# Performance work log

Measured on AMD Instinct MI355X. Metric: run time of the kernel, lower is better.

Reference implementation:

```python
import jax, jax.numpy as jnp
import numpy as np

N = 50000        # nodes
E = 800000       # edges (before self-loops)
IN_C = 256
OUT_C = 64
HEADS = 4
NEG_SLOPE = 0.2  # PyG GATConv default


def setup_inputs() -> dict:
    key = jax.random.key(0)
    k0, k1, k2, k3, k4 = jax.random.split(key, 5)
    x = jax.random.normal(k0, (N, IN_C), jnp.float32)
    edge_index = jax.random.randint(k1, (2, E), 0, N, dtype=jnp.int32)
    W = jax.random.normal(k2, (IN_C, HEADS * OUT_C), jnp.float32) * (1.0 / np.sqrt(IN_C))
    att_src = jax.random.normal(k3, (HEADS, OUT_C), jnp.float32) * 0.1
    att_dst = jax.random.normal(k4, (HEADS, OUT_C), jnp.float32) * 0.1
    bias = jnp.zeros((OUT_C,), jnp.float32)
    return {"x": x, "edge_index": edge_index, "W": W,
            "att_src": att_src, "att_dst": att_dst, "bias": bias}


def reference(x, edge_index, W, att_src, att_dst, bias):
    n = x.shape[0]
    # PyG GATConv default add_self_loops=True
    loop = jnp.arange(n, dtype=edge_index.dtype)
    src = jnp.concatenate([edge_index[0], loop])  # [E+N]
    dst = jnp.concatenate([edge_index[1], loop])  # [E+N]

    h = (x @ W).reshape(n, HEADS, OUT_C)                    # [N,H,C]
    a_src = jnp.einsum('nhc,hc->nh', h, att_src)            # [N,H]
    a_dst = jnp.einsum('nhc,hc->nh', h, att_dst)            # [N,H]

    e = jax.nn.leaky_relu(a_src[src] + a_dst[dst], NEG_SLOPE)   # [E',H]
    # segment softmax over edges grouped by destination node
    m = jax.lax.stop_gradient(jax.ops.segment_max(e, dst, num_segments=n))  # [N,H]
    ex = jnp.exp(e - m[dst])
    denom = jax.ops.segment_sum(ex, dst, num_segments=n)    # [N,H]
    alpha = ex / (denom[dst] + 1e-16)                       # [E',H]

    out = jax.ops.segment_sum(alpha[:, :, None] * h[src], dst, num_segments=n)  # [N,H,C]
    # concat=False -> mean over heads, then bias
    return out.mean(axis=1) + bias
```

## Files before the change

kernel.cpp:

```cpp
#include <hip/hip_runtime.h>
#include <hip/hip_bf16.h>

#define INC   256
#define HEADS 4
#define OUTC  64
#define NEG_SLOPE 0.2f
#define CAP   5120
#define EPB_A 2048

typedef __attribute__((ext_vector_type(8))) short  fragA;
typedef __attribute__((ext_vector_type(4))) float  f32x4;

__device__ __forceinline__ float bf2f(unsigned short u) {
    union { unsigned int i; float f; } v; v.i = ((unsigned int)u) << 16; return v.f;
}
__device__ __forceinline__ unsigned short f2bf(float x) {
    __hip_bfloat16 b = __float2bfloat16(x);
    return *reinterpret_cast<unsigned short*>(&b);
}

__global__ __launch_bounds__(256) void wt_zero_kernel(const float* __restrict__ W,
                                                      unsigned short* __restrict__ Wt,
                                                      int* __restrict__ btail, int nbuck)
{
    int idx = blockIdx.x * 256 + threadIdx.x;
    int k = idx >> 8, c = idx & 255;
    Wt[c * 256 + k] = f2bf(W[k * 256 + c]);
    if (idx < nbuck) btail[idx] = 0;
}

__global__ __launch_bounds__(256, 2) void gemm_passA(
    const float* __restrict__ A,
    const unsigned short* __restrict__ Wt,
    const float* __restrict__ att_src,
    const float* __restrict__ att_dst,
    unsigned short* __restrict__ H2,
    float* __restrict__ a_srcO,
    float* __restrict__ a_dstO,
    int M,
    const int* __restrict__ src, const int* __restrict__ dst,
    int* __restrict__ btail,
    int2* __restrict__ bucketbuf,
    int E, int nbA)
{
    __shared__ __align__(16) unsigned short As[64 * 256];
    const int tid = threadIdx.x;

    if ((int)blockIdx.x < nbA) {
        char* sm = (char*)As;
        int* lhist = (int*)sm;
        int* lrankc = (int*)(sm + 1024);
        int* gbase  = (int*)(sm + 2048);
        lhist[tid] = 0; lrankc[tid] = 0;
        __syncthreads();
        int e0 = blockIdx.x * EPB_A;
        int e1 = e0 + EPB_A; if (e1 > E) e1 = E;
        for (int e = e0 + tid; e < e1; e += 256)
            atomicAdd(&lhist[dst[e] >> 8], 1);
        __syncthreads();
        {
            int c = lhist[tid];
            gbase[tid] = (c > 0) ? atomicAdd(&btail[tid], c) : 0;
        }
        __syncthreads();
        for (int e = e0 + tid; e < e1; e += 256) {
            int s = src[e], d = dst[e];
            int b = d >> 8;
            int r = atomicAdd(&lrankc[b], 1);
            bucketbuf[(size_t)b * CAP + gbase[b] + r] = make_int2(s, d);
        }
        return;
    }

    const int lane = tid & 63;
    const int wave = tid >> 6;
    const int row0 = ((int)blockIdx.x - nbA) * 64;
    const int g   = lane >> 4;
    const int r16 = lane & 15;

    fragA b[4][8];
    {
        const unsigned short* wp = Wt + (size_t)(wave * 64) * 256;
        #pragma unroll
        for (int nn = 0; nn < 4; ++nn)
            #pragma unroll
            for (int kk = 0; kk < 8; ++kk)
                b[nn][kk] = *(const fragA*)(wp + (size_t)(nn * 16 + r16) * 256 + kk * 32 + g * 8);
    }

    #pragma unroll
    for (int i = 0; i < 16; ++i) {
        int f   = i * 256 + tid;
        int row = f >> 6;
        int q   = f & 63;
        int gr  = row0 + row;
        float4 v = (gr < M) ? *(const float4*)(A + (size_t)gr * INC + q * 4)
                            : make_float4(0.f, 0.f, 0.f, 0.f);
        ushort4 u;
        u.x = f2bf(v.x); u.y = f2bf(v.y); u.z = f2bf(v.z); u.w = f2bf(v.w);
        int byte = (row << 9) + (q << 3);
        byte ^= (row & 7) << 4;
        *(ushort4*)((char*)As + byte) = u;
    }
    __syncthreads();

    f32x4 acc[4][4] = {};
    #pragma unroll
    for (int kk = 0; kk < 8; ++kk) {
        fragA a[4];
        #pragma unroll
        for (int m = 0; m < 4; ++m) {
            int row  = m * 16 + r16;
            int byte = (row << 9) + ((kk * 32 + g * 8) << 1);
            byte ^= (row & 7) << 4;
            a[m] = *(const fragA*)((const char*)As + byte);
        }
        #pragma unroll
        for (int m = 0; m < 4; ++m)
            #pragma unroll
            for (int nn = 0; nn < 4; ++nn)
                acc[m][nn] = __builtin_amdgcn_mfma_f32_16x16x32_bf16(
                    a[m], b[nn][kk], acc[m][nn], 0, 0, 0);
    }

    #pragma unroll
    for (int m = 0; m < 4; ++m) {
        #pragma unroll
        for (int nn = 0; nn < 4; ++nn) {
            int gcol = wave * 64 + nn * 16 + r16;
            #pragma unroll
            for (int r = 0; r < 4; ++r) {
                int grow = row0 + m * 16 + g * 4 + r;
                if (grow < M)
                    H2[(size_t)grow * (HEADS * OUTC) + gcol] = f2bf(acc[m][nn][r]);
            }
        }
    }

    {
        float as_att[4], ad_att[4];
        #pragma unroll
        for (int nn = 0; nn < 4; ++nn) {
            as_att[nn] = att_src[wave * 64 + nn * 16 + r16];
            ad_att[nn] = att_dst[wave * 64 + nn * 16 + r16];
        }
        float sv[4][4], dv[4][4];
        #pragma unroll
        for (int m = 0; m < 4; ++m)
            #pragma unroll
            for (int r = 0; r < 4; ++r) {
                float s = 0.f, d = 0.f;
                #pragma unroll
                for (int nn = 0; nn < 4; ++nn) {
                    s = fmaf(acc[m][nn][r], as_att[nn], s);
                    d = fmaf(acc[m][nn][r], ad_att[nn], d);
                }
                sv[m][r] = s; dv[m][r] = d;
            }
        #pragma unroll
        for (int off = 1; off < 16; off <<= 1) {
            #pragma unroll
            for (int m = 0; m < 4; ++m)
                #pragma unroll
                for (int r = 0; r < 4; ++r) {
                    sv[m][r] += __shfl_xor(sv[m][r], off, 64);
                    dv[m][r] += __shfl_xor(dv[m][r], off, 64);
                }
        }
        #pragma unroll
        for (int m = 0; m < 4; ++m)
            #pragma unroll
            for (int r = 0; r < 4; ++r) {
                if (r16 == m * 4 + r) {
                    int grow = row0 + m * 16 + g * 4 + r;
                    if (grow < M) {
                        a_srcO[(size_t)grow * HEADS + wave] = sv[m][r];
                        a_dstO[(size_t)grow * HEADS + wave] = dv[m][r];
                    }
                }
            }
    }
}

__global__ __launch_bounds__(256) void passB_kernel(const int2* __restrict__ bucketbuf,
                                                    const int* __restrict__ btail,
                                                    int* __restrict__ offsets,
                                                    int* __restrict__ esrc,
                                                    int N, int E)
{
    __shared__ int lcnt[256];
    __shared__ int red[256];
    __shared__ unsigned short lrank[CAP];
    const int b = blockIdx.x, t = threadIdx.x;

    int s0 = 0;
    for (int j = t; j < b; j += 256) s0 += btail[j];
    red[t] = s0;
    __syncthreads();
    for (int off = 128; off > 0; off >>= 1) {
        if (t < off) red[t] += red[t + off];
        __syncthreads();
    }
    const int baseg = red[0];
    const int cnt = btail[b];
    __syncthreads();

    lcnt[t] = 0;
    __syncthreads();
    const int2* bb = bucketbuf + (size_t)b * CAP;
    for (int i = t; i < cnt; i += 256)
        lrank[i] = (unsigned short)atomicAdd(&lcnt[bb[i].y & 255], 1);
    __syncthreads();

    int v = lcnt[t];
    red[t] = v;
    __syncthreads();
    for (int off = 1; off < 256; off <<= 1) {
        int x = (t >= off) ? red[t - off] : 0;
        __syncthreads();
        red[t] += x;
        __syncthreads();
    }
    int excl = red[t] - v;
    lcnt[t] = excl;
    int node = b * 256 + t;
    if (node < N) offsets[node] = baseg + excl;
    if (b == 0 && t == 0) offsets[N] = E;
    __syncthreads();

    for (int i = t; i < cnt; i += 256) {
        int2 sd = bb[i];
        int slot = baseg + lcnt[sd.y & 255] + lrank[i];
        esrc[slot] = sd.x;
    }
}

__global__ __launch_bounds__(128) void fused_agg_kernel(
    const unsigned short* __restrict__ h2,
    const float* __restrict__ a_src,
    const float* __restrict__ a_dst,
    const int*   __restrict__ offsets,
    const int*   __restrict__ esrc,
    const float* __restrict__ bias,
    float*       __restrict__ out,
    int n)
{
    int i    = (int)((blockIdx.x * blockDim.x + threadIdx.x) >> 6);
    int lane = threadIdx.x & 63;
    if (i >= n) return;
    const int h  = lane >> 4;
    const int cg = lane & 15;

    const float ad = a_dst[(size_t)i * HEADS + h];
    const unsigned short* h2p = h2 + lane * 4;

    float acc0, acc1, acc2, acc3, l;
    {
        float as = a_src[(size_t)i * HEADS + h];
        float e = as + ad; e = e > 0.f ? e : NEG_SLOPE * e;
        float p = __expf(e);
        ushort4 v = *(const ushort4*)(h2p + (size_t)i * 256);
        l = p;
        acc0 = p * bf2f(v.x);
        acc1 = p * bf2f(v.y);
        acc2 = p * bf2f(v.z);
        acc3 = p * bf2f(v.w);
    }

#define EDGE_BODY(S, AS)                                                     \
    {                                                                        \
        float e_ = (AS) + ad; e_ = e_ > 0.f ? e_ : NEG_SLOPE * e_;           \
        float p_ = __expf(e_);                                               \
        ushort4 v_ = *(const ushort4*)(h2p + (size_t)(S) * 256);             \
        l += p_;                                                             \
        acc0 = fmaf(p_, bf2f(v_.x), acc0);                                   \
        acc1 = fmaf(p_, bf2f(v_.y), acc1);                                   \
        acc2 = fmaf(p_, bf2f(v_.z), acc2);                                   \
        acc3 = fmaf(p_, bf2f(v_.w), acc3);                                   \
    }

    int beg = offsets[i], end = offsets[i + 1];
    int j = beg;
    for (; j < end && (j & 3); ++j) {
        int s = esrc[j];
        float as = a_src[(size_t)s * HEADS + h];
        EDGE_BODY(s, as);
    }
    for (; j + 3 < end; j += 4) {
        int4 ea = *(const int4*)(esrc + j);
        float as0 = a_src[(size_t)ea.x * HEADS + h];
        float as1 = a_src[(size_t)ea.y * HEADS + h];
        float as2 = a_src[(size_t)ea.z * HEADS + h];
        float as3 = a_src[(size_t)ea.w * HEADS + h];
        ushort4 v0 = *(const ushort4*)(h2p + (size_t)ea.x * 256);
        ushort4 v1 = *(const ushort4*)(h2p + (size_t)ea.y * 256);
        ushort4 v2 = *(const ushort4*)(h2p + (size_t)ea.z * 256);
        ushort4 v3 = *(const ushort4*)(h2p + (size_t)ea.w * 256);
        float e0 = as0 + ad; e0 = e0 > 0.f ? e0 : NEG_SLOPE * e0; float p0 = __expf(e0);
        float e1 = as1 + ad; e1 = e1 > 0.f ? e1 : NEG_SLOPE * e1; float p1 = __expf(e1);
        float e2 = as2 + ad; e2 = e2 > 0.f ? e2 : NEG_SLOPE * e2; float p2 = __expf(e2);
        float e3 = as3 + ad; e3 = e3 > 0.f ? e3 : NEG_SLOPE * e3; float p3 = __expf(e3);
        l += (p0 + p1) + (p2 + p3);
        acc0 = fmaf(p0, bf2f(v0.x), acc0);
        acc1 = fmaf(p0, bf2f(v0.y), acc1);
        acc2 = fmaf(p0, bf2f(v0.z), acc2);
        acc3 = fmaf(p0, bf2f(v0.w), acc3);
        acc0 = fmaf(p1, bf2f(v1.x), acc0);
        acc1 = fmaf(p1, bf2f(v1.y), acc1);
        acc2 = fmaf(p1, bf2f(v1.z), acc2);
        acc3 = fmaf(p1, bf2f(v1.w), acc3);
        acc0 = fmaf(p2, bf2f(v2.x), acc0);
        acc1 = fmaf(p2, bf2f(v2.y), acc1);
        acc2 = fmaf(p2, bf2f(v2.z), acc2);
        acc3 = fmaf(p2, bf2f(v2.w), acc3);
        acc0 = fmaf(p3, bf2f(v3.x), acc0);
        acc1 = fmaf(p3, bf2f(v3.y), acc1);
        acc2 = fmaf(p3, bf2f(v3.z), acc2);
        acc3 = fmaf(p3, bf2f(v3.w), acc3);
    }
    for (; j < end; ++j) {
        int s = esrc[j];
        float as = a_src[(size_t)s * HEADS + h];
        EDGE_BODY(s, as);
    }
#undef EDGE_BODY

    float inv = 1.f / (l + 1e-16f);
    float r0 = acc0 * inv, r1 = acc1 * inv, r2 = acc2 * inv, r3 = acc3 * inv;

    r0 += __shfl_xor(r0, 16, 64); r0 += __shfl_xor(r0, 32, 64);
    r1 += __shfl_xor(r1, 16, 64); r1 += __shfl_xor(r1, 32, 64);
    r2 += __shfl_xor(r2, 16, 64); r2 += __shfl_xor(r2, 32, 64);
    r3 += __shfl_xor(r3, 16, 64); r3 += __shfl_xor(r3, 32, 64);

    if (lane < 16) {
        float4 b4 = *(const float4*)(bias + cg * 4);
        float4 o;
        o.x = 0.25f * r0 + b4.x;
        o.y = 0.25f * r1 + b4.y;
        o.z = 0.25f * r2 + b4.z;
        o.w = 0.25f * r3 + b4.w;
        *(float4*)(out + (size_t)i * OUTC + cg * 4) = o;
    }
}

extern "C" void kernel_launch(void* const* d_in, const int* in_sizes, int n_in,
                              void* d_out, int out_size, void* d_ws, size_t ws_size,
                              hipStream_t stream)
{
    (void)n_in; (void)out_size; (void)ws_size;
    const float* x       = (const float*)d_in[0];
    const int*   edge    = (const int*)d_in[1];
    const float* W       = (const float*)d_in[2];
    const float* att_src = (const float*)d_in[3];
    const float* att_dst = (const float*)d_in[4];
    const float* bias    = (const float*)d_in[5];
    float* out = (float*)d_out;

    const int N = in_sizes[0] / INC;
    const int E = in_sizes[1] / 2;
    const int* srcA = edge;
    const int* dstA = edge + E;
    const int nbuck = (N + 255) / 256;
    const int nbA   = (E + EPB_A - 1) / EPB_A;

    char* ws = (char*)d_ws;
    unsigned short* h2 = (unsigned short*)ws; ws += (size_t)N * (HEADS * OUTC) * sizeof(unsigned short);
    unsigned short* Wt = (unsigned short*)ws; ws += (size_t)256 * 256 * sizeof(unsigned short);
    float* a_src  = (float*)ws; ws += (size_t)N * HEADS * sizeof(float);
    float* a_dst  = (float*)ws; ws += (size_t)N * HEADS * sizeof(float);
    int* offsets  = (int*)ws;   ws += (size_t)(N + 1) * sizeof(int) + 12;
    int* btail    = (int*)ws;   ws += (size_t)256 * sizeof(int);
    int2* bucketbuf = (int2*)ws; ws += (size_t)nbuck * CAP * sizeof(int2);
    int* esrc     = (int*)ws;   ws += (size_t)E * sizeof(int);

    wt_zero_kernel<<<256, 256, 0, stream>>>(W, Wt, btail, nbuck);

    gemm_passA<<<nbA + (N + 63) / 64, 256, 0, stream>>>(
        x, Wt, att_src, att_dst, h2, a_src, a_dst, N,
        srcA, dstA, btail, bucketbuf, E, nbA);

    passB_kernel<<<nbuck, 256, 0, stream>>>(bucketbuf, btail, offsets, esrc, N, E);

    fused_agg_kernel<<<(N + 1) / 2, 128, 0, stream>>>(h2, a_src, a_dst, offsets, esrc,
                                                      bias, out, N);
}
```

Measured before the change: 135.7 us.

## Replace global atomic bucket reservation with separate histogram and scan kernels

The per-block destination histogram and the global atomicAdd on the bucket tails are split out of the fused GEMM/bucketing kernel. They become a histogram kernel plus a per-bucket exclusive scan kernel, so each bucketing block gets precomputed, deterministic base offsets. This removes the contended global atomics and one pass over dst from the bucketing blocks. In exchange it adds two kernel launches, an extra read of dst, and blockhist/blockbase traffic, all on the critical path before the GEMM launch.

```diff
diff --git a/kernel.cpp b/kernel.cpp
--- a/kernel.cpp
+++ b/kernel.cpp
@@ -19,14 +19,47 @@
     return *reinterpret_cast<unsigned short*>(&b);
 }
 
-__global__ __launch_bounds__(256) void wt_zero_kernel(const float* __restrict__ W,
-                                                      unsigned short* __restrict__ Wt,
-                                                      int* __restrict__ btail, int nbuck)
+__global__ __launch_bounds__(256) void wt_kernel(const float* __restrict__ W,
+                                                 unsigned short* __restrict__ Wt)
 {
     int idx = blockIdx.x * 256 + threadIdx.x;
     int k = idx >> 8, c = idx & 255;
     Wt[c * 256 + k] = f2bf(W[k * 256 + c]);
-    if (idx < nbuck) btail[idx] = 0;
+}
+
+__global__ __launch_bounds__(256) void passA1_kernel(const int* __restrict__ dst,
+                                                     int* __restrict__ blockhist,
+                                                     int E)
+{
+    __shared__ int lh[256];
+    const int t = threadIdx.x, blk = blockIdx.x;
+    lh[t] = 0;
+    __syncthreads();
+    int e0 = blk * EPB_A;
+    int e1 = e0 + EPB_A; if (e1 > E) e1 = E;
+    for (int e = e0 + t; e < e1; e += 256)
+        atomicAdd(&lh[dst[e] >> 8], 1);
+    __syncthreads();
+    blockhist[blk * 256 + t] = lh[t];
+}
+
+__global__ __launch_bounds__(512) void scanb_kernel(const int* __restrict__ blockhist,
+                                                    int* __restrict__ blockbase,
+                                                    int* __restrict__ btail, int nbA)
+{
+    __shared__ int tmp[512];
+    const int t = threadIdx.x, b = blockIdx.x;
+    int v = (t < nbA) ? blockhist[t * 256 + b] : 0;
+    tmp[t] = v;
+    __syncthreads();
+    for (int off = 1; off < 512; off <<= 1) {
+        int x = (t >= off) ? tmp[t - off] : 0;
+        __syncthreads();
+        tmp[t] += x;
+        __syncthreads();
+    }
+    if (t < nbA) blockbase[t * 256 + b] = tmp[t] - v;
+    if (t == nbA - 1) btail[b] = tmp[t];
 }
 
 __global__ __launch_bounds__(256, 2) void gemm_passA(
@@ -39,7 +72,7 @@
     float* __restrict__ a_dstO,
     int M,
     const int* __restrict__ src, const int* __restrict__ dst,
-    int* __restrict__ btail,
+    const int* __restrict__ blockbase,
     int2* __restrict__ bucketbuf,
     int E, int nbA)
 {
@@ -48,26 +81,18 @@
 
     if ((int)blockIdx.x < nbA) {
         char* sm = (char*)As;
-        int* lhist = (int*)sm;
-        int* lrankc = (int*)(sm + 1024);
-        int* gbase  = (int*)(sm + 2048);
-        lhist[tid] = 0; lrankc[tid] = 0;
+        int* lrankc = (int*)sm;
+        int* lbase  = (int*)(sm + 1024);
+        lrankc[tid] = 0;
+        lbase[tid]  = blockbase[(size_t)blockIdx.x * 256 + tid];
         __syncthreads();
         int e0 = blockIdx.x * EPB_A;
         int e1 = e0 + EPB_A; if (e1 > E) e1 = E;
-        for (int e = e0 + tid; e < e1; e += 256)
-            atomicAdd(&lhist[dst[e] >> 8], 1);
-        __syncthreads();
-        {
-            int c = lhist[tid];
-            gbase[tid] = (c > 0) ? atomicAdd(&btail[tid], c) : 0;
-        }
-        __syncthreads();
         for (int e = e0 + tid; e < e1; e += 256) {
             int s = src[e], d = dst[e];
             int b = d >> 8;
             int r = atomicAdd(&lrankc[b], 1);
-            bucketbuf[(size_t)b * CAP + gbase[b] + r] = make_int2(s, d);
+            bucketbuf[(size_t)b * CAP + lbase[b] + r] = make_int2(s, d);
         }
         return;
     }
@@ -371,14 +396,19 @@
     float* a_dst  = (float*)ws; ws += (size_t)N * HEADS * sizeof(float);
     int* offsets  = (int*)ws;   ws += (size_t)(N + 1) * sizeof(int) + 12;
     int* btail    = (int*)ws;   ws += (size_t)256 * sizeof(int);
+    int* blockhist= (int*)ws;   ws += (size_t)nbA * 256 * sizeof(int);
+    int* blockbase= (int*)ws;   ws += (size_t)nbA * 256 * sizeof(int);
     int2* bucketbuf = (int2*)ws; ws += (size_t)nbuck * CAP * sizeof(int2);
     int* esrc     = (int*)ws;   ws += (size_t)E * sizeof(int);
 
-    wt_zero_kernel<<<256, 256, 0, stream>>>(W, Wt, btail, nbuck);
+    wt_kernel<<<256, 256, 0, stream>>>(W, Wt);
+
+    passA1_kernel<<<nbA, 256, 0, stream>>>(dstA, blockhist, E);
+    scanb_kernel<<<256, 512, 0, stream>>>(blockhist, blockbase, btail, nbA);
 
     gemm_passA<<<nbA + (N + 63) / 64, 256, 0, stream>>>(
         x, Wt, att_src, att_dst, h2, a_src, a_dst, N,
-        srcA, dstA, btail, bucketbuf, E, nbA);
+        srcA, dstA, blockbase, bucketbuf, E, nbA);
 
     passB_kernel<<<nbuck, 256, 0, stream>>>(bucketbuf, btail, offsets, esrc, N, E);
 
```

New measurement: 136.5 us. About the same (+0.6%).

## Load GEMM A fragments directly from global, drop LDS staging and preloaded B

Applied to the files above, without the earlier changes.

The GEMM part of the fused kernel no longer converts a 64x256 tile of x into swizzled LDS. Each wave instead loads and converts its A fragments straight from global memory per k-step, and loads W fragments per k-step rather than preloading all 32 into registers. This removes the LDS tile, its barrier and most register pressure, so more blocks can be resident once the min-blocks launch bound is dropped. The cost is that all 4 waves of a block re-read the same A rows from global/L2 with strided 32-byte loads. Edges per histogram block are also doubled to cut block count and global atomics.

```diff
diff --git a/kernel.cpp b/kernel.cpp
--- a/kernel.cpp
+++ b/kernel.cpp
@@ -6,7 +6,7 @@
 #define OUTC  64
 #define NEG_SLOPE 0.2f
 #define CAP   5120
-#define EPB_A 2048
+#define EPB_A 4096
 
 typedef __attribute__((ext_vector_type(8))) short  fragA;
 typedef __attribute__((ext_vector_type(4))) float  f32x4;
@@ -18,18 +18,28 @@
     __hip_bfloat16 b = __float2bfloat16(x);
     return *reinterpret_cast<unsigned short*>(&b);
 }
+__device__ __forceinline__ fragA load_cvt(const float* __restrict__ p) {
+    float4 lo = *(const float4*)p;
+    float4 hi = *(const float4*)(p + 4);
+    fragA f;
+    f[0] = (short)f2bf(lo.x); f[1] = (short)f2bf(lo.y);
+    f[2] = (short)f2bf(lo.z); f[3] = (short)f2bf(lo.w);
+    f[4] = (short)f2bf(hi.x); f[5] = (short)f2bf(hi.y);
+    f[6] = (short)f2bf(hi.z); f[7] = (short)f2bf(hi.w);
+    return f;
+}
 
 __global__ __launch_bounds__(256) void wt_zero_kernel(const float* __restrict__ W,
                                                       unsigned short* __restrict__ Wt,
-                                                      int* __restrict__ btail, int nbuck)
+                                                      int* __restrict__ btail)
 {
     int idx = blockIdx.x * 256 + threadIdx.x;
     int k = idx >> 8, c = idx & 255;
     Wt[c * 256 + k] = f2bf(W[k * 256 + c]);
-    if (idx < nbuck) btail[idx] = 0;
-}
-
-__global__ __launch_bounds__(256, 2) void gemm_passA(
+    if (idx < 256) btail[idx] = 0;
+}
+
+__global__ __launch_bounds__(256) void gemm_passA(
     const float* __restrict__ A,
     const unsigned short* __restrict__ Wt,
     const float* __restrict__ att_src,
@@ -43,14 +53,12 @@
     int2* __restrict__ bucketbuf,
     int E, int nbA)
 {
-    __shared__ __align__(16) unsigned short As[64 * 256];
+    __shared__ int lhist[256];
+    __shared__ int lrankc[256];
+    __shared__ int gbase[256];
     const int tid = threadIdx.x;
 
     if ((int)blockIdx.x < nbA) {
-        char* sm = (char*)As;
-        int* lhist = (int*)sm;
-        int* lrankc = (int*)(sm + 1024);
-        int* gbase  = (int*)(sm + 2048);
         lhist[tid] = 0; lrankc[tid] = 0;
         __syncthreads();
         int e0 = blockIdx.x * EPB_A;
@@ -78,49 +86,31 @@
     const int g   = lane >> 4;
     const int r16 = lane & 15;
 
-    fragA b[4][8];
-    {
-        const unsigned short* wp = Wt + (size_t)(wave * 64) * 256;
-        #pragma unroll
-        for (int nn = 0; nn < 4; ++nn)
-            #pragma unroll
-            for (int kk = 0; kk < 8; ++kk)
-                b[nn][kk] = *(const fragA*)(wp + (size_t)(nn * 16 + r16) * 256 + kk * 32 + g * 8);
-    }
-
+    const float* ar[4];
     #pragma unroll
-    for (int i = 0; i < 16; ++i) {
-        int f   = i * 256 + tid;
-        int row = f >> 6;
-        int q   = f & 63;
-        int gr  = row0 + row;
-        float4 v = (gr < M) ? *(const float4*)(A + (size_t)gr * INC + q * 4)
-                            : make_float4(0.f, 0.f, 0.f, 0.f);
-        ushort4 u;
-        u.x = f2bf(v.x); u.y = f2bf(v.y); u.z = f2bf(v.z); u.w = f2bf(v.w);
-        int byte = (row << 9) + (q << 3);
-        byte ^= (row & 7) << 4;
-        *(ushort4*)((char*)As + byte) = u;
-    }
-    __syncthreads();
+    for (int m = 0; m < 4; ++m) {
+        int row = row0 + m * 16 + r16;
+        if (row > M - 1) row = M - 1;
+        ar[m] = A + (size_t)row * INC;
+    }
+    const unsigned short* wp = Wt + (size_t)(wave * 64) * 256;
 
     f32x4 acc[4][4] = {};
     #pragma unroll
     for (int kk = 0; kk < 8; ++kk) {
-        fragA a[4];
-        #pragma unroll
-        for (int m = 0; m < 4; ++m) {
-            int row  = m * 16 + r16;
-            int byte = (row << 9) + ((kk * 32 + g * 8) << 1);
-            byte ^= (row & 7) << 4;
-            a[m] = *(const fragA*)((const char*)As + byte);
-        }
+        fragA a[4], b[4];
+        #pragma unroll
+        for (int m = 0; m < 4; ++m)
+            a[m] = load_cvt(ar[m] + kk * 32 + g * 8);
+        #pragma unroll
+        for (int nn = 0; nn < 4; ++nn)
+            b[nn] = *(const fragA*)(wp + (size_t)(nn * 16 + r16) * 256 + kk * 32 + g * 8);
         #pragma unroll
         for (int m = 0; m < 4; ++m)
             #pragma unroll
             for (int nn = 0; nn < 4; ++nn)
                 acc[m][nn] = __builtin_amdgcn_mfma_f32_16x16x32_bf16(
-                    a[m], b[nn][kk], acc[m][nn], 0, 0, 0);
+                    a[m], b[nn], acc[m][nn], 0, 0, 0);
     }
 
     #pragma unroll
@@ -374,7 +364,7 @@
     int2* bucketbuf = (int2*)ws; ws += (size_t)nbuck * CAP * sizeof(int2);
     int* esrc     = (int*)ws;   ws += (size_t)E * sizeof(int);
 
-    wt_zero_kernel<<<256, 256, 0, stream>>>(W, Wt, btail, nbuck);
+    wt_zero_kernel<<<256, 256, 0, stream>>>(W, Wt, btail);
 
     gemm_passA<<<nbA + (N + 63) / 64, 256, 0, stream>>>(
         x, Wt, att_src, att_dst, h2, a_src, a_dst, N,
```

New measurement: 144.3 us. +6.4%, slower.
